# Kernel optimization log

Measured on AMD Instinct MI355X. Metric: run time of the kernel, lower is better.

Reference implementation:

```python
import jax, jax.numpy as jnp
import numpy as np

N_USERS = 100000
N_ITEMS = 50000
EMB = 64
E_U = 1600000
E_I = 800000
EPS = 1e-12
NEG_SLOPE = 0.01  # torch F.leaky_relu default


def _spmm(rows, cols, vals, x, n):
    # sparse.mm(adj, x): out[r] += vals[e] * x[cols[e]] for each edge e with rows[e]==r
    return jax.ops.segment_sum(vals[:, None] * x[cols], rows, num_segments=n)


def _l2norm(x):
    # F.normalize(x, p=2, dim=1)
    n = jnp.sqrt(jnp.sum(x * x, axis=1, keepdims=True))
    return x / jnp.maximum(n, EPS)


def setup_inputs() -> dict:
    key = jax.random.key(0)
    ks = jax.random.split(key, 16)
    inp = {
        'user_emb': 0.01 * jax.random.normal(ks[0], (N_USERS, EMB), jnp.float32),
        'item_emb': 0.01 * jax.random.normal(ks[1], (N_ITEMS, EMB), jnp.float32),
        'Wu0': jax.random.normal(ks[2], (EMB, EMB), jnp.float32) / np.sqrt(EMB),
        'bu0': jnp.zeros((EMB,), jnp.float32),
        'Wu1': jax.random.normal(ks[3], (EMB, EMB), jnp.float32) / np.sqrt(EMB),
        'bu1': jnp.zeros((EMB,), jnp.float32),
        'Wi0': jax.random.normal(ks[4], (EMB, EMB), jnp.float32) / np.sqrt(EMB),
        'bi0': jnp.zeros((EMB,), jnp.float32),
        'Wi1': jax.random.normal(ks[5], (EMB, EMB), jnp.float32) / np.sqrt(EMB),
        'bi1': jnp.zeros((EMB,), jnp.float32),
        'u_rows': jax.random.randint(ks[6], (E_U,), 0, N_USERS, jnp.int32),
        'u_cols': jax.random.randint(ks[7], (E_U,), 0, N_USERS, jnp.int32),
        'u_vals': jax.random.uniform(ks[8], (E_U,), jnp.float32) / 16.0,
        'i_rows': jax.random.randint(ks[9], (E_I,), 0, N_ITEMS, jnp.int32),
        'i_cols': jax.random.randint(ks[10], (E_I,), 0, N_ITEMS, jnp.int32),
        'i_vals': jax.random.uniform(ks[11], (E_I,), jnp.float32) / 16.0,
    }
    return inp


def reference(user_emb, item_emb, Wu0, bu0, Wu1, bu1, Wi0, bi0, Wi1, bi1,
              u_rows, u_cols, u_vals, i_rows, i_cols, i_vals):
    u = user_emb
    i = item_emb
    u_w = [(Wu0, bu0), (Wu1, bu1)]
    i_w = [(Wi0, bi0), (Wi1, bi1)]
    for l in range(2):
        Wu, bu = u_w[l]
        Wi, bi = i_w[l]
        u = _spmm(u_rows, u_cols, u_vals, u, N_USERS)
        u = jax.nn.leaky_relu(u @ Wu.T + bu, NEG_SLOPE)
        u = _l2norm(u)  # dropout p=0 -> identity
        i = _spmm(i_rows, i_cols, i_vals, i, N_ITEMS)
        i = jax.nn.leaky_relu(i @ Wi.T + bi, NEG_SLOPE)
        i = _l2norm(i)
    return (u, i)
```

## Files before the change

kernel.cpp:

```cpp
#include <hip/hip_runtime.h>
#include <hip/hip_bf16.h>
#include <math.h>

#define EMB 64
#define CAPB 3584
#define CHUNK 4096

typedef __attribute__((ext_vector_type(8))) short bf16x8;
typedef __attribute__((ext_vector_type(4))) float f32x4;

__device__ __forceinline__ ushort bf16_rne(float f) {
    uint u = __float_as_uint(f);
    return (ushort)((u + 0x7fffu + ((u >> 16) & 1u)) >> 16);
}

__device__ __forceinline__ uint bf16_pack2(float a, float b) {
    return (uint)bf16_rne(a) | ((uint)bf16_rne(b) << 16);
}


__device__ __forceinline__ void bin_body(
    const int* __restrict__ rows, const int* __restrict__ cols,
    const float* __restrict__ vals, int nE, int B, int RPB,
    int* gcur, int2* __restrict__ binned, int blk,
    int* cnt, int* sstart, int* lbase, int2* rec, ushort* bkt) {
    int t = threadIdx.x;
    for (int i = t; i < B; i += 256) cnt[i] = 0;
    __syncthreads();
    int c0 = blk * CHUNK;
    int ntot = nE - c0; if (ntot > CHUNK) ntot = CHUNK;
    int bs[16];
#pragma unroll
    for (int j = 0; j < 16; ++j) {
        int idx = c0 + t + j * 256;
        int bsv = -1;
        if (idx < nE) {
            int row = rows[idx];
            int b = row / RPB;
            int inrow = row - b * RPB;
            int slot = atomicAdd(&cnt[b], 1);
            bsv = (b << 21) | (inrow << 13) | slot;
        }
        bs[j] = bsv;
    }
    __syncthreads();
    for (int i = t; i < B; i += 256) {
        int c = cnt[i];
        lbase[i] = c ? atomicAdd(&gcur[i * 16], c) : 0;
    }
    if (t < 64) {
        int carry = 0;
        int nseg = B >> 6;
        for (int seg = 0; seg < nseg; ++seg) {
            int i = seg * 64 + t;
            int v = cnt[i];
            int s = v;
#pragma unroll
            for (int d = 1; d < 64; d <<= 1) {
                int u2 = __shfl_up(s, d);
                if (t >= d) s += u2;
            }
            sstart[i] = carry + s - v;
            carry += __shfl(s, 63);
        }
    }
    __syncthreads();
#pragma unroll
    for (int j = 0; j < 16; ++j) {
        int idx = c0 + t + j * 256;
        if (idx >= nE) continue;
        int bsv = bs[j];
        int b = bsv >> 21, inrow = (bsv >> 13) & 0xFF, slot = bsv & 0x1FFF;
        int col = cols[idx];
        float v = vals[idx];
        int li = sstart[b] + slot;
        rec[li] = make_int2(col | (inrow << 17), __float_as_int(v));
        bkt[li] = (ushort)b;
    }
    __syncthreads();
    for (int i = t; i < ntot; i += 256) {
        int b = bkt[i];
        int pos = lbase[b] + (i - sstart[b]);
        if (pos < CAPB)
            binned[(size_t)b * CAPB + pos] = rec[i];
    }
}

__global__ __launch_bounds__(256) void prep(
    const int* __restrict__ u_rows, const int* __restrict__ u_cols,
    const float* __restrict__ u_vals, int eu, int BU, int RPBU,
    int* gcurU, int2* __restrict__ binnedU, int nbU,
    const int* __restrict__ i_rows, const int* __restrict__ i_cols,
    const float* __restrict__ i_vals, int ei, int BI, int RPBI,
    int* gcurI, int2* __restrict__ binnedI, int nbI,
    const float4* __restrict__ embU, ushort* __restrict__ xbU, long n4u,
    const float4* __restrict__ embI, ushort* __restrict__ xbI, long n4i,
    int nbCast,
    const float4* __restrict__ W0s, ushort* __restrict__ W0d,
    const float4* __restrict__ W1s, ushort* __restrict__ W1d,
    const float4* __restrict__ W2s, ushort* __restrict__ W2d,
    const float4* __restrict__ W3s, ushort* __restrict__ W3d) {
    __shared__ int2 rec[CHUNK];
    __shared__ ushort bkt[CHUNK];
    __shared__ int cnt[512];
    __shared__ int sstart[512];
    __shared__ int lbase[512];
    int b = blockIdx.x;
    if (b < nbU) {
        bin_body(u_rows, u_cols, u_vals, eu, BU, RPBU, gcurU, binnedU, b,
                 cnt, sstart, lbase, rec, bkt);
        return;
    }
    b -= nbU;
    if (b < nbI) {
        bin_body(i_rows, i_cols, i_vals, ei, BI, RPBI, gcurI, binnedI, b,
                 cnt, sstart, lbase, rec, bkt);
        return;
    }
    b -= nbI;
    if (b < nbCast) {
        long tot = n4u + n4i;
        long base = (long)b * 1024 + threadIdx.x;
#pragma unroll
        for (int k = 0; k < 4; ++k) {
            long i = base + k * 256;
            if (i >= tot) return;
            const float4* a; ushort* o; long j;
            if (i < n4u) { a = embU; o = xbU; j = i; }
            else { a = embI; o = xbI; j = i - n4u; }
            float4 v = a[j];
            ushort4 r;
            r.x = bf16_rne(v.x); r.y = bf16_rne(v.y); r.z = bf16_rne(v.z); r.w = bf16_rne(v.w);
            *(ushort4*)(o + j * 4) = r;
        }
        return;
    }
    b -= nbCast;
    {
        const float4* src = (b == 0) ? W0s : (b == 1) ? W1s : (b == 2) ? W2s : W3s;
        ushort* dst = (b == 0) ? W0d : (b == 1) ? W1d : (b == 2) ? W2d : W3d;
        int t = threadIdx.x;
        float4 v0 = src[t * 4 + 0], v1 = src[t * 4 + 1];
        float4 v2 = src[t * 4 + 2], v3 = src[t * 4 + 3];
        uint4 o0, o1;
        o0.x = bf16_pack2(v0.x, v0.y); o0.y = bf16_pack2(v0.z, v0.w);
        o0.z = bf16_pack2(v1.x, v1.y); o0.w = bf16_pack2(v1.z, v1.w);
        o1.x = bf16_pack2(v2.x, v2.y); o1.y = bf16_pack2(v2.z, v2.w);
        o1.z = bf16_pack2(v3.x, v3.y); o1.w = bf16_pack2(v3.z, v3.w);
        ((uint4*)dst)[t * 2 + 0] = o0;
        ((uint4*)dst)[t * 2 + 1] = o1;
    }
}


__global__ __launch_bounds__(256) void finalize_csr(
    const int2* __restrict__ binnedU, const int* __restrict__ gcurU, int RPBU, int nu,
    uint* __restrict__ ccvpU, int2* __restrict__ offseU, int BU,
    const int2* __restrict__ binnedI, const int* __restrict__ gcurI, int RPBI, int ni,
    uint* __restrict__ ccvpI, int2* __restrict__ offseI) {
    __shared__ int2 rec[CAPB];
    __shared__ int cnt_r[256];
    __shared__ int excl[257];
    __shared__ int curs[256];
    int b = blockIdx.x;
    const int2* binned; const int* gcur; int RPB; int n; uint* ccvp; int2* offse;
    if (b < BU) {
        binned = binnedU; gcur = gcurU; RPB = RPBU; n = nu; ccvp = ccvpU; offse = offseU;
    } else {
        b -= BU;
        binned = binnedI; gcur = gcurI; RPB = RPBI; n = ni; ccvp = ccvpI; offse = offseI;
    }
    int t = threadIdx.x;
    int r0 = b * RPB;
    int nrows = n - r0; if (nrows > RPB) nrows = RPB;
    if (nrows <= 0) return;
    int cnt = gcur[b * 16];
    if (cnt > CAPB) cnt = CAPB;
    const int2* src = binned + (size_t)b * CAPB;
    int B0 = b * CAPB;
    cnt_r[t] = 0;
    __syncthreads();
    for (int p = t; p < cnt; p += 256) {
        int2 r = src[p];
        rec[p] = r;
        atomicAdd(&cnt_r[(r.x >> 17) & 0xFF], 1);
    }
    __syncthreads();
    if (t < 64) {
        int carry = 0;
#pragma unroll
        for (int seg = 0; seg < 4; ++seg) {
            int i = seg * 64 + t;
            int v = cnt_r[i];
            int s = v;
#pragma unroll
            for (int d = 1; d < 64; d <<= 1) {
                int u2 = __shfl_up(s, d);
                if (t >= d) s += u2;
            }
            excl[i] = carry + s - v;
            carry += __shfl(s, 63);
        }
        if (t == 0) excl[256] = carry;
    }
    __syncthreads();
    curs[t] = excl[t];
    if (t < nrows) offse[r0 + t] = make_int2(B0 + excl[t], B0 + excl[t + 1]);
    __syncthreads();
    for (int p = t; p < cnt; p += 256) {
        int2 r = rec[p];
        int inrow = (r.x >> 17) & 0xFF;
        int slot = atomicAdd(&curs[inrow], 1);
        float v = __int_as_float(r.y);
        uint v15 = ((uint)bf16_rne(v)) & 0x7FFFu;
        ccvp[B0 + slot] = (uint)(r.x & 0x1FFFF) | (v15 << 17);
    }
}


__global__ __launch_bounds__(256, 6) void spmm_mfma(
    const int2* __restrict__ offseU, const uint* __restrict__ ccvU,
    const ushort* __restrict__ xu, const ushort* __restrict__ Wu, const float* __restrict__ bu,
    float* __restrict__ yfu, ushort* __restrict__ ybu, int nu, int ntU,
    const int2* __restrict__ offseI, const uint* __restrict__ ccvI,
    const ushort* __restrict__ xi, const ushort* __restrict__ Wi, const float* __restrict__ bi,
    float* __restrict__ yfi, ushort* __restrict__ ybi, int ni) {
    __shared__ ushort wt[64 * 72];
    __shared__ ushort xt[4 * 16 * 72];
    int tid = threadIdx.x;
    int lane = tid & 63, wid = tid >> 6;
    int q = lane & 15, g = lane >> 4;
    int tile = blockIdx.x;
    const int2* offse; const uint* ccv; const ushort* x; const ushort* W; const float* bv;
    float* yf; ushort* yb; int n;
    if (tile < ntU) {
        offse = offseU; ccv = ccvU; x = xu; W = Wu; bv = bu; yf = yfu; yb = ybu; n = nu;
    } else {
        tile -= ntU;
        offse = offseI; ccv = ccvI; x = xi; W = Wi; bv = bi; yf = yfi; yb = ybi; n = ni;
    }
    {
        int r = tid >> 2, c = (tid & 3) * 16;
        uint4 v0 = ((const uint4*)W)[tid * 2 + 0];
        uint4 v1 = ((const uint4*)W)[tid * 2 + 1];
        *(uint4*)(wt + r * 72 + c) = v0;
        *(uint4*)(wt + r * 72 + c + 8) = v1;
    }
    float bias[4];
#pragma unroll
    for (int t = 0; t < 4; ++t) bias[t] = bv[16 * t + q];
    __syncthreads();

    const uint2* xv2 = (const uint2*)x;
    ushort* xw = xt + wid * (16 * 72);
    int rowW = (tile << 6) + wid * 16;

#pragma unroll
    for (int j = 0; j < 4; ++j) {
        int rr = j * 4 + g;
        int row = rowW + rr;
        float av[4] = {0.f, 0.f, 0.f, 0.f};
        if (row < n) {
            int2 se = offse[row];
            int s = se.x, e = se.y;
            for (int p = s; p < e; p += 8) {
                uint ed[8];
                uint2 gx[8];
#pragma unroll
                for (int k = 0; k < 8; ++k) {
                    int idx = p + k;
                    idx = (idx < e) ? idx : (e - 1);
                    ed[k] = ccv[idx];
                }
#pragma unroll
                for (int k = 0; k < 8; ++k)
                    gx[k] = xv2[(size_t)(ed[k] & 0x1FFFFu) * 16 + q];
#pragma unroll
                for (int k = 0; k < 8; ++k) {
                    float v = (p + k < e) ? __uint_as_float((ed[k] >> 17) << 16) : 0.f;
                    av[0] = fmaf(v, __uint_as_float(gx[k].x << 16), av[0]);
                    av[1] = fmaf(v, __uint_as_float(gx[k].x & 0xffff0000u), av[1]);
                    av[2] = fmaf(v, __uint_as_float(gx[k].y << 16), av[2]);
                    av[3] = fmaf(v, __uint_as_float(gx[k].y & 0xffff0000u), av[3]);
                }
            }
        }
        uint p0 = (uint)bf16_rne(av[0]) | ((uint)bf16_rne(av[1]) << 16);
        uint p1 = (uint)bf16_rne(av[2]) | ((uint)bf16_rne(av[3]) << 16);
        *(uint2*)(xw + rr * 72 + q * 4) = make_uint2(p0, p1);
    }
    __syncthreads();

    f32x4 ac0 = {0.f, 0.f, 0.f, 0.f}, ac1 = ac0, ac2 = ac0, ac3 = ac0;
#pragma unroll
    for (int ks = 0; ks < 2; ++ks) {
        bf16x8 af = *(const bf16x8*)(xw + q * 72 + g * 8 + ks * 32);
        bf16x8 b0 = *(const bf16x8*)(wt + (q +  0) * 72 + g * 8 + ks * 32);
        bf16x8 b1 = *(const bf16x8*)(wt + (q + 16) * 72 + g * 8 + ks * 32);
        bf16x8 b2 = *(const bf16x8*)(wt + (q + 32) * 72 + g * 8 + ks * 32);
        bf16x8 b3 = *(const bf16x8*)(wt + (q + 48) * 72 + g * 8 + ks * 32);
        ac0 = __builtin_amdgcn_mfma_f32_16x16x32_bf16(af, b0, ac0, 0, 0, 0);
        ac1 = __builtin_amdgcn_mfma_f32_16x16x32_bf16(af, b1, ac1, 0, 0, 0);
        ac2 = __builtin_amdgcn_mfma_f32_16x16x32_bf16(af, b2, ac2, 0, 0, 0);
        ac3 = __builtin_amdgcn_mfma_f32_16x16x32_bf16(af, b3, ac3, 0, 0, 0);
    }

    float dv[4][4];
    float ss[4] = {0.f, 0.f, 0.f, 0.f};
#pragma unroll
    for (int t = 0; t < 4; ++t) {
        f32x4 a = (t == 0) ? ac0 : (t == 1) ? ac1 : (t == 2) ? ac2 : ac3;
#pragma unroll
        for (int r = 0; r < 4; ++r) {
            float d = a[r] + bias[t];
            d = (d > 0.f) ? d : 0.01f * d;
            dv[t][r] = d;
            ss[r] = fmaf(d, d, ss[r]);
        }
    }
#pragma unroll
    for (int r = 0; r < 4; ++r) {
        float s2 = ss[r];
        s2 += __shfl_xor(s2, 1);
        s2 += __shfl_xor(s2, 2);
        s2 += __shfl_xor(s2, 4);
        s2 += __shfl_xor(s2, 8);
        float scl = 1.0f / fmaxf(sqrtf(s2), 1e-12f);
        int orow = rowW + g * 4 + r;
        if (orow < n) {
#pragma unroll
            for (int t = 0; t < 4; ++t) {
                float outv = dv[t][r] * scl;
                size_t cidx = (size_t)orow * EMB + 16 * t + q;
                if (yb) yb[cidx] = bf16_rne(outv);
                else    yf[cidx] = outv;
            }
        }
    }
}


extern "C" void kernel_launch(void* const* d_in, const int* in_sizes, int n_in,
                              void* d_out, int out_size, void* d_ws, size_t ws_size,
                              hipStream_t stream) {
    const float* user_emb = (const float*)d_in[0];
    const float* item_emb = (const float*)d_in[1];
    const float* Wu0 = (const float*)d_in[2];
    const float* bu0 = (const float*)d_in[3];
    const float* Wu1 = (const float*)d_in[4];
    const float* bu1 = (const float*)d_in[5];
    const float* Wi0 = (const float*)d_in[6];
    const float* bi0 = (const float*)d_in[7];
    const float* Wi1 = (const float*)d_in[8];
    const float* bi1 = (const float*)d_in[9];
    const int*   u_rows = (const int*)d_in[10];
    const int*   u_cols = (const int*)d_in[11];
    const float* u_vals = (const float*)d_in[12];
    const int*   i_rows = (const int*)d_in[13];
    const int*   i_cols = (const int*)d_in[14];
    const float* i_vals = (const float*)d_in[15];

    const int nu = in_sizes[0] / EMB;
    const int ni = in_sizes[1] / EMB;
    const int eu = in_sizes[10];
    const int ei = in_sizes[13];

    const int BU = 512, BI = 256;
    const int RPBU = (nu + BU - 1) / BU;
    const int RPBI = (ni + BI - 1) / BI;

    float* out_u = (float*)d_out;
    float* out_i = out_u + (size_t)nu * EMB;

    size_t o = 0;
    char* wsb = (char*)d_ws;
    auto carve = [&](size_t bytes) -> void* {
        void* p = wsb + o;
        o += (bytes + 255) & ~(size_t)255;
        return p;
    };
    ushort* xbu0 = (ushort*)carve((size_t)nu * EMB * 2);
    ushort* xbi0 = (ushort*)carve((size_t)ni * EMB * 2);
    int2* binnedU = (int2*)carve((size_t)BU * CAPB * 8);
    int2* binnedI = (int2*)carve((size_t)BI * CAPB * 8);
    uint* ccvpU = (uint*)carve((size_t)BU * CAPB * 4);
    uint* ccvpI = (uint*)carve((size_t)BI * CAPB * 4);
    ushort* xbu1 = (ushort*)carve((size_t)nu * EMB * 2);
    ushort* xbi1 = (ushort*)carve((size_t)ni * EMB * 2);
    int2* offseU = (int2*)carve((size_t)nu * 8);
    int2* offseI = (int2*)carve((size_t)ni * 8);
    ushort* wpkU0 = (ushort*)carve(4096 * 2);
    ushort* wpkI0 = (ushort*)carve(4096 * 2);
    ushort* wpkU1 = (ushort*)carve(4096 * 2);
    ushort* wpkI1 = (ushort*)carve(4096 * 2);
    int*  gcur  = (int*)carve((size_t)(BU + BI) * 16 * 4);
    int*  gcurU = gcur;
    int*  gcurI = gcur + (size_t)BU * 16;
    (void)ws_size;

    hipMemsetAsync(gcur, 0, (size_t)(BU + BI) * 16 * 4, stream);
    {
        int nbU = (eu + CHUNK - 1) / CHUNK;
        int nbI = (ei + CHUNK - 1) / CHUNK;
        long n4u = (long)nu * EMB / 4, n4i = (long)ni * EMB / 4;
        int nbCast = (int)((n4u + n4i + 1023) / 1024);
        prep<<<nbU + nbI + nbCast + 4, 256, 0, stream>>>(
            u_rows, u_cols, u_vals, eu, BU, RPBU, gcurU, binnedU, nbU,
            i_rows, i_cols, i_vals, ei, BI, RPBI, gcurI, binnedI, nbI,
            (const float4*)user_emb, xbu0, n4u,
            (const float4*)item_emb, xbi0, n4i, nbCast,
            (const float4*)Wu0, wpkU0, (const float4*)Wi0, wpkI0,
            (const float4*)Wu1, wpkU1, (const float4*)Wi1, wpkI1);
    }
    finalize_csr<<<BU + BI, 256, 0, stream>>>(
        binnedU, gcurU, RPBU, nu, ccvpU, offseU, BU,
        binnedI, gcurI, RPBI, ni, ccvpI, offseI);

    int ntU = (nu + 63) >> 6, ntI = (ni + 63) >> 6;
    spmm_mfma<<<ntU + ntI, 256, 0, stream>>>(
        offseU, ccvpU, xbu0, wpkU0, bu0, nullptr, xbu1, nu, ntU,
        offseI, ccvpI, xbi0, wpkI0, bi0, nullptr, xbi1, ni);
    spmm_mfma<<<ntU + ntI, 256, 0, stream>>>(
        offseU, ccvpU, xbu1, wpkU1, bu1, out_u, nullptr, nu, ntU,
        offseI, ccvpI, xbi1, wpkI1, bi1, out_i, nullptr, ni);
}
```

Measured before the change: 161.3 us.

## Software-pipeline edge index loads across row batches in SpMM gather loop

The gather loop now prefetches the next batch of packed column/value words while issuing the feature gathers for the current batch, carrying the prefetch across row boundaries. Row offsets for all 16 rows are loaded once per wave and broadcast with shuffles instead of each row loading its own. This aims to hide the dependent-load latency of index-then-gather. The extra registers led to lowering the launch-bounds occupancy hint from 6 to 4, which trades some latency hiding from parallel waves.

```diff
diff --git a/kernel.cpp b/kernel.cpp
--- a/kernel.cpp
+++ b/kernel.cpp
@@ -218,7 +218,7 @@
 }
 
 
-__global__ __launch_bounds__(256, 6) void spmm_mfma(
+__global__ __launch_bounds__(256, 4) void spmm_mfma(
     const int2* __restrict__ offseU, const uint* __restrict__ ccvU,
     const ushort* __restrict__ xu, const ushort* __restrict__ Wu, const float* __restrict__ bu,
     float* __restrict__ yfu, ushort* __restrict__ ybu, int nu, int ntU,
@@ -255,36 +255,63 @@
     ushort* xw = xt + wid * (16 * 72);
     int rowW = (tile << 6) + wid * 16;
 
+    int2 se = make_int2(0, 0);
+    {
+        int r16 = rowW + lane;
+        if (lane < 16 && r16 < n) se = offse[r16];
+    }
+    int Sa[4], Ea[4];
 #pragma unroll
     for (int j = 0; j < 4; ++j) {
+        Sa[j] = __shfl(se.x, j * 4 + g);
+        Ea[j] = __shfl(se.y, j * 4 + g);
+    }
+
+    uint edC[8], edN[8];
+    {
+        int sn = Sa[0], en = Ea[0];
+        int safe = (en > sn) ? en - 1 : 0;
+#pragma unroll
+        for (int k = 0; k < 8; ++k) {
+            int ii = sn + k;
+            edC[k] = ccv[(ii < en) ? ii : safe];
+        }
+    }
+#pragma unroll
+    for (int j = 0; j < 4; ++j) {
+        int s = Sa[j], e = Ea[j];
+        int sN = (j < 3) ? Sa[j + 1] : 0;
+        int eN = (j < 3) ? Ea[j + 1] : 0;
+        float av[4] = {0.f, 0.f, 0.f, 0.f};
+        int nb = (e - s + 7) >> 3; if (nb < 1) nb = 1;
+        int p = s;
+        for (int b = 0; b < nb; ++b, p += 8) {
+            bool lastb = (b + 1 >= nb);
+            int pn = lastb ? sN : (p + 8);
+            int en = lastb ? eN : e;
+            int sn = lastb ? sN : s;
+            uint2 gx[8];
+#pragma unroll
+            for (int k = 0; k < 8; ++k)
+                gx[k] = xv2[(size_t)(edC[k] & 0x1FFFFu) * 16 + q];
+            int safeN = (en > sn) ? en - 1 : 0;
+#pragma unroll
+            for (int k = 0; k < 8; ++k) {
+                int ii = pn + k;
+                edN[k] = ccv[(ii < en) ? ii : safeN];
+            }
+#pragma unroll
+            for (int k = 0; k < 8; ++k) {
+                float v = (p + k < e) ? __uint_as_float((edC[k] >> 17) << 16) : 0.f;
+                av[0] = fmaf(v, __uint_as_float(gx[k].x << 16), av[0]);
+                av[1] = fmaf(v, __uint_as_float(gx[k].x & 0xffff0000u), av[1]);
+                av[2] = fmaf(v, __uint_as_float(gx[k].y << 16), av[2]);
+                av[3] = fmaf(v, __uint_as_float(gx[k].y & 0xffff0000u), av[3]);
+            }
+#pragma unroll
+            for (int k = 0; k < 8; ++k) edC[k] = edN[k];
+        }
         int rr = j * 4 + g;
-        int row = rowW + rr;
-        float av[4] = {0.f, 0.f, 0.f, 0.f};
-        if (row < n) {
-            int2 se = offse[row];
-            int s = se.x, e = se.y;
-            for (int p = s; p < e; p += 8) {
-                uint ed[8];
-                uint2 gx[8];
-#pragma unroll
-                for (int k = 0; k < 8; ++k) {
-                    int idx = p + k;
-                    idx = (idx < e) ? idx : (e - 1);
-                    ed[k] = ccv[idx];
-                }
-#pragma unroll
-                for (int k = 0; k < 8; ++k)
-                    gx[k] = xv2[(size_t)(ed[k] & 0x1FFFFu) * 16 + q];
-#pragma unroll
-                for (int k = 0; k < 8; ++k) {
-                    float v = (p + k < e) ? __uint_as_float((ed[k] >> 17) << 16) : 0.f;
-                    av[0] = fmaf(v, __uint_as_float(gx[k].x << 16), av[0]);
-                    av[1] = fmaf(v, __uint_as_float(gx[k].x & 0xffff0000u), av[1]);
-                    av[2] = fmaf(v, __uint_as_float(gx[k].y << 16), av[2]);
-                    av[3] = fmaf(v, __uint_as_float(gx[k].y & 0xffff0000u), av[3]);
-                }
-            }
-        }
         uint p0 = (uint)bf16_rne(av[0]) | ((uint)bf16_rne(av[1]) << 16);
         uint p1 = (uint)bf16_rne(av[2]) | ((uint)bf16_rne(av[3]) << 16);
         *(uint2*)(xw + rr * 72 + q * 4) = make_uint2(p0, p1);
```

After: 158.7 us (median of 2 runs). About the same (-1.7%).
